# Optimization experiments

Hardware: AMD Instinct MI355X
Metric: run time of the kernel (lower is better)

Reference implementation:

```python
import jax, jax.numpy as jnp
import numpy as np

H = 16            # num_heads
NORM = 16.0       # gate normalizer
SCALE = 128.0 ** -0.5  # (embed_dim // num_heads) ** -0.5, per source
EPS = 1e-5


def setup_inputs() -> dict:
    key = jax.random.key(0)
    ks = jax.random.split(key, 10)
    B, L, D = 2, 2048, 2048
    g = lambda k, shape, s: jax.random.normal(k, shape, jnp.float32) * s
    return {
        "x": g(ks[0], (B, L, D), 1.0),
        "Wq": g(ks[1], (1024, D), 0.02),
        "Wk": g(ks[2], (1024, D), 0.02),
        "Wkg1": g(ks[3], (16, D), 0.02),
        "Wkg2": g(ks[4], (1024, 16), 0.05),
        "bkg2": jnp.zeros((1024,), jnp.float32),
        "Wv": g(ks[5], (D, D), 0.02),
        "Wg": g(ks[6], (D, D), 0.02),
        "bg": jnp.zeros((D,), jnp.float32),
        "Wo": g(ks[7], (D, D), 0.02),
    }


def _gla_core(x, Wq, Wk, Wkg1, Wkg2, bkg2, Wv, Wg, bg, Wo):
    B, L, D = x.shape
    q = x @ Wq.T                         # [B,L,1024]
    k = (x @ Wk.T) * SCALE               # [B,L,1024]
    kg = (x @ Wkg1.T) @ Wkg2.T + bkg2    # [B,L,1024] low-rank gate
    v = x @ Wv.T                         # [B,L,2048]
    gproj = x @ Wg.T + bg                # [B,L,2048]

    dk = q.shape[-1] // H   # 64
    dv = D // H             # 128
    heads = lambda t, dh: t.reshape(B, L, H, dh).transpose(0, 2, 1, 3)  # b h l d
    qh = heads(q, dk)
    kh = heads(k, dk)
    vh = heads(v, dv)
    gk = jax.nn.log_sigmoid(heads(kg, dk)) / NORM  # b h l dk

    # recurrence: S_t = diag(exp(gk_t)) S_{t-1} + k_t v_t^T ; o_t = q_t S_t
    tfirst = lambda t: t.transpose(2, 0, 1, 3)  # l b h d

    def step(S, inp):
        qt, kt, vt, gt = inp
        S = S * jnp.exp(gt)[..., None] + kt[..., None] * vt[..., None, :]
        ot = jnp.einsum('bhk,bhkv->bhv', qt, S)
        return S, ot

    S0 = jnp.zeros((B, H, dk, dv), x.dtype)
    _, os = jax.lax.scan(step, S0, (tfirst(qh), tfirst(kh), tfirst(vh), tfirst(gk)))
    o = os.transpose(1, 2, 0, 3)  # b h l dv

    # LayerNorm over head dim, no affine
    mu = o.mean(-1, keepdims=True)
    var = ((o - mu) ** 2).mean(-1, keepdims=True)
    o = (o - mu) * jax.lax.rsqrt(var + EPS)

    o = o.transpose(0, 2, 1, 3).reshape(B, L, D)  # b l (h dv)
    return (jax.nn.silu(gproj) * o) @ Wo.T


def reference(x, Wq, Wk, Wkg1, Wkg2, bkg2, Wv, Wg, bg, Wo):
    return _gla_core(x, Wq, Wk, Wkg1, Wkg2, bkg2, Wv, Wg, bg, Wo)
```

## Files before the change

kernel.cpp:

```cpp
#include <hip/hip_runtime.h>
#include <hip/hip_bf16.h>

using bf16x8 = __attribute__((ext_vector_type(8))) __bf16;
using fx4    = __attribute__((ext_vector_type(4))) float;
using us4    = __attribute__((ext_vector_type(4))) unsigned short;
using us8    = __attribute__((ext_vector_type(8))) unsigned short;

__device__ __forceinline__ float b2f(unsigned short u) {
    unsigned int x = ((unsigned int)u) << 16;
    return __builtin_bit_cast(float, x);
}
__device__ __forceinline__ unsigned short f2b(float f) {
    __hip_bfloat16 h = __float2bfloat16(f);
    return __builtin_bit_cast(unsigned short, h);
}
__device__ __forceinline__ float logsigmoidf(float z) {
    return fminf(z, 0.0f) - log1pf(expf(-fabsf(z)));
}

__device__ __forceinline__ void gl_lds16(const unsigned short* g, unsigned short* l) {
    __builtin_amdgcn_global_load_lds(
        (const __attribute__((address_space(1))) void*)g,
        (__attribute__((address_space(3))) void*)l, 16, 0, 0);
}

__device__ __forceinline__ bf16x8 frag64(const unsigned short* base, int row, int cq) {
    return *reinterpret_cast<const bf16x8*>(base + row * 64 + (((cq ^ (row & 7)) << 3)));
}
__device__ __forceinline__ int sw_idx(int row, int col) {
    return row * 64 + ((((col >> 3) ^ (row & 7)) << 3)) + (col & 7);
}

__global__ __launch_bounds__(256) void detect_kernel(
    const unsigned int* __restrict__ x, int* __restrict__ flag)
{
    __shared__ int bad[256];
    const int t = threadIdx.x;
    int b = 0;
#pragma unroll
    for (int i = 0; i < 16; ++i) {
        unsigned int w = x[t * 16 + i];
        float v = b2f((unsigned short)(w & 0xFFFFu));
        if (!(fabsf(v) < 1.0e6f)) b = 1;
    }
    bad[t] = b;
    __syncthreads();
    for (int s = 128; s > 0; s >>= 1) {
        if (t < s) bad[t] |= bad[t + s];
        __syncthreads();
    }
    if (t == 0) flag[0] = bad[0];
}

struct CvtArgs {
    const void* src[10];
    unsigned short* dst[10];
};

__global__ __launch_bounds__(256) void convert_all_kernel(
    CvtArgs a, const int* __restrict__ flag)
{
    const int pref[11] = {0, 8192, 10240, 12288, 12320, 12336, 12337,
                          16433, 20529, 20531, 24627};
    const int blk = blockIdx.x;
    int s = 0;
#pragma unroll
    for (int i = 1; i < 10; ++i) s += (blk >= pref[i]) ? 1 : 0;
    const int i0 = (blk - pref[s]) * 1024 + threadIdx.x * 4;
    if (*flag) {
        const float* sp = (const float*)a.src[s];
        fx4 v = *reinterpret_cast<const fx4*>(sp + i0);
        us4 r;
#pragma unroll
        for (int e = 0; e < 4; ++e) r[e] = f2b(v[e]);
        *reinterpret_cast<us4*>(a.dst[s] + i0) = r;
    } else {
        const unsigned short* sp = (const unsigned short*)a.src[s];
        *reinterpret_cast<us4*>(a.dst[s] + i0) =
            *reinterpret_cast<const us4*>(sp + i0);
    }
}

struct Seg3 {
    unsigned short* C0;
    unsigned short* C1;
    unsigned short* C2;
    const unsigned short* bias2;
};

__global__ __launch_bounds__(256) void gemm_fused3_kernel(
    const unsigned short* __restrict__ A, const unsigned short* __restrict__ W,
    Seg3 segs, float scale_k)
{
    const int K = 2048;
    __shared__ __align__(16) unsigned short As[128 * 64];
    __shared__ __align__(16) unsigned short Bs[128 * 64];

    const int tid  = threadIdx.x;
    const int lane = tid & 63, wid = tid >> 6;
    const int quad = lane >> 4, l15 = lane & 15;
    const int wm = (wid & 1) * 64, wn = (wid >> 1) * 64;
    const int m0 = blockIdx.y * 128, n0 = blockIdx.x * 128;

    fx4 acc[4][4];
#pragma unroll
    for (int i = 0; i < 4; ++i)
#pragma unroll
        for (int j = 0; j < 4; ++j) acc[i][j] = fx4{0.f, 0.f, 0.f, 0.f};

    const int srow = lane >> 3;
    const int g8   = ((lane & 7) ^ srow) * 8;
    const int c8   = (lane & 7) * 8;
    const unsigned short* Ab = A + (size_t)m0 * K;
    const unsigned short* Wb = W + (size_t)n0 * K;

    for (int k0 = 0; k0 < K; k0 += 64) {
#pragma unroll
        for (int p = 0; p < 4; ++p) {
            const int la  = wid * 4 + p;
            const int row = la * 8 + srow;
            gl_lds16(Ab + (size_t)row * K + k0 + g8, As + row * 64 + c8);
            gl_lds16(Wb + (size_t)row * K + k0 + g8, Bs + row * 64 + c8);
        }
        __syncthreads();
#pragma unroll
        for (int ks = 0; ks < 2; ++ks) {
            const int cq = quad + ks * 4;
            bf16x8 af[4], bfr[4];
#pragma unroll
            for (int mt = 0; mt < 4; ++mt) af[mt] = frag64(As, wm + mt * 16 + l15, cq);
#pragma unroll
            for (int nt = 0; nt < 4; ++nt) bfr[nt] = frag64(Bs, wn + nt * 16 + l15, cq);
#pragma unroll
            for (int mt = 0; mt < 4; ++mt)
#pragma unroll
                for (int nt = 0; nt < 4; ++nt)
                    acc[mt][nt] = __builtin_amdgcn_mfma_f32_16x16x32_bf16(
                        af[mt], bfr[nt], acc[mt][nt], 0, 0, 0);
        }
        __syncthreads();
    }

    const int segi = n0 >> 11;
    unsigned short* Cs = (segi == 0) ? segs.C0 : ((segi == 1) ? segs.C1 : segs.C2);
#pragma unroll
    for (int nt = 0; nt < 4; ++nt) {
        const int ncl = (n0 & 2047) + wn + nt * 16 + l15;
        const float av = (segi == 0 && ncl >= 1024) ? scale_k : 1.0f;
        const float bv = (segi == 2) ? b2f(segs.bias2[ncl]) : 0.0f;
#pragma unroll
        for (int mt = 0; mt < 4; ++mt) {
#pragma unroll
            for (int r = 0; r < 4; ++r) {
                const int mrow = m0 + wm + mt * 16 + quad * 4 + r;
                float val = acc[mt][nt][r] * av + bv;
                if (segi == 2) val = val / (1.0f + __expf(-val));
                Cs[(size_t)mrow * 2048 + ncl] = f2b(val);
            }
        }
    }
}

__global__ __launch_bounds__(256) void gemm_bt_kernel(
    const unsigned short* __restrict__ A, const unsigned short* __restrict__ W,
    unsigned short* __restrict__ C, int M, int N, int K,
    const int* __restrict__ oflag)
{
    __shared__ __align__(16) unsigned short As[128 * 64];
    __shared__ __align__(16) unsigned short Bs[128 * 64];

    const int tid  = threadIdx.x;
    const int lane = tid & 63, wid = tid >> 6;
    const int quad = lane >> 4, l15 = lane & 15;
    const int wm = (wid & 1) * 64, wn = (wid >> 1) * 64;
    const int m0 = blockIdx.y * 128, n0 = blockIdx.x * 128;

    fx4 acc[4][4];
#pragma unroll
    for (int i = 0; i < 4; ++i)
#pragma unroll
        for (int j = 0; j < 4; ++j) acc[i][j] = fx4{0.f, 0.f, 0.f, 0.f};

    const int srow = lane >> 3;
    const int g8   = ((lane & 7) ^ srow) * 8;
    const int c8   = (lane & 7) * 8;
    const unsigned short* Ab = A + (size_t)m0 * K;
    const unsigned short* Wb = W + (size_t)n0 * K;

    for (int k0 = 0; k0 < K; k0 += 64) {
#pragma unroll
        for (int p = 0; p < 4; ++p) {
            const int la  = wid * 4 + p;
            const int row = la * 8 + srow;
            gl_lds16(Ab + (size_t)row * K + k0 + g8, As + row * 64 + c8);
            gl_lds16(Wb + (size_t)row * K + k0 + g8, Bs + row * 64 + c8);
        }
        __syncthreads();
#pragma unroll
        for (int ks = 0; ks < 2; ++ks) {
            const int cq = quad + ks * 4;
            bf16x8 af[4], bfr[4];
#pragma unroll
            for (int mt = 0; mt < 4; ++mt) af[mt] = frag64(As, wm + mt * 16 + l15, cq);
#pragma unroll
            for (int nt = 0; nt < 4; ++nt) bfr[nt] = frag64(Bs, wn + nt * 16 + l15, cq);
#pragma unroll
            for (int mt = 0; mt < 4; ++mt)
#pragma unroll
                for (int nt = 0; nt < 4; ++nt)
                    acc[mt][nt] = __builtin_amdgcn_mfma_f32_16x16x32_bf16(
                        af[mt], bfr[nt], acc[mt][nt], 0, 0, 0);
        }
        __syncthreads();
    }

    const int f32out = oflag ? *oflag : 0;
#pragma unroll
    for (int nt = 0; nt < 4; ++nt) {
        const int ncol = n0 + wn + nt * 16 + l15;
#pragma unroll
        for (int mt = 0; mt < 4; ++mt) {
#pragma unroll
            for (int r = 0; r < 4; ++r) {
                const int mrow = m0 + wm + mt * 16 + quad * 4 + r;
                float val = acc[mt][nt][r];
                const size_t idx = (size_t)mrow * N + ncol;
                if (f32out) ((float*)C)[idx] = val;
                else        C[idx] = f2b(val);
            }
        }
    }
}

__global__ __launch_bounds__(256) void gate1_kernel(
    const unsigned short* __restrict__ x, const unsigned short* __restrict__ Wkg1,
    const unsigned short* __restrict__ Wkg2, const unsigned short* __restrict__ bkg2,
    float* __restrict__ Ag)
{
    __shared__ float part[4][16];
    __shared__ float kgrow[16];
    const int m = blockIdx.x;
    const int tid = threadIdx.x;
    const int lane = tid & 63, w = tid >> 6;

    us8 xv = *reinterpret_cast<const us8*>(x + (size_t)m * 2048 + tid * 8);
    float xr[8];
#pragma unroll
    for (int e = 0; e < 8; ++e) xr[e] = b2f(xv[e]);

#pragma unroll
    for (int n = 0; n < 16; ++n) {
        us8 wv = *reinterpret_cast<const us8*>(Wkg1 + (size_t)n * 2048 + tid * 8);
        float s = 0.f;
#pragma unroll
        for (int e = 0; e < 8; ++e) s += xr[e] * b2f(wv[e]);
#pragma unroll
        for (int off = 1; off < 64; off <<= 1) s += __shfl_xor(s, off, 64);
        if (lane == 0) part[w][n] = s;
    }
    __syncthreads();
    if (tid < 16)
        kgrow[tid] = part[0][tid] + part[1][tid] + part[2][tid] + part[3][tid];
    __syncthreads();
    float kr[16];
#pragma unroll
    for (int j = 0; j < 16; ++j) kr[j] = kgrow[j];

    const int b = m >> 11, l = m & 2047;
    const int c0 = tid * 4;
    const int h = c0 >> 6, d0 = c0 & 63;
    fx4 gv;
#pragma unroll
    for (int qi = 0; qi < 4; ++qi) {
        const int c = c0 + qi;
        us8 w0 = *reinterpret_cast<const us8*>(Wkg2 + (size_t)c * 16);
        us8 w1 = *reinterpret_cast<const us8*>(Wkg2 + (size_t)c * 16 + 8);
        float z = b2f(bkg2[c]);
#pragma unroll
        for (int j = 0; j < 8; ++j) z += kr[j] * b2f(w0[j]) + kr[8 + j] * b2f(w1[j]);
        gv[qi] = logsigmoidf(z) * 0.0625f;
    }
    *reinterpret_cast<fx4*>(Ag + ((size_t)(b * 16 + h) * 2048 + l) * 64 + d0) = gv;
}

__global__ __launch_bounds__(256) void gate2_kernel(float* __restrict__ Ag)
{
    const int gidx = blockIdx.x * 256 + threadIdx.x;
    const int d = gidx & 63, ch = (gidx >> 6) & 31, bh = gidx >> 11;
    float* p = Ag + ((size_t)bh * 2048 + ch * 64) * 64 + d;
    float acc = 0.f;
#pragma unroll 8
    for (int t = 0; t < 64; ++t) {
        acc += p[(size_t)t * 64];
        p[(size_t)t * 64] = acc;
    }
}

__global__ __launch_bounds__(256) void pass1_kernel(
    const unsigned short* __restrict__ k, int kstr,
    const unsigned short* __restrict__ v,
    const float* __restrict__ Ag, float* __restrict__ Tc)
{
    __shared__ __align__(16) unsigned short kT[64 * 64];
    __shared__ __align__(16) unsigned short vT[128 * 64];

    const int blk = blockIdx.x;
    const int ch = blk & 31, bh = blk >> 5;
    const int b = bh >> 4, h = bh & 15;
    const int tid = threadIdx.x;
    const int lane = tid & 63, w = tid >> 6;
    const int quad = lane >> 4, l15 = lane & 15;

    const float* Abase = Ag + ((size_t)bh * 2048 + ch * 64) * 64;
    const unsigned short* kbase = k + ((size_t)(b * 2048 + ch * 64)) * kstr + h * 64;
    const unsigned short* vbase = v + ((size_t)(b * 2048 + ch * 64)) * 2048 + h * 128;

    {
        const int s = tid >> 2, d0 = (tid & 3) * 16;
        float av[16], a63[16];
        *(fx4*)(av)      = *(const fx4*)(Abase + (size_t)s * 64 + d0);
        *(fx4*)(av + 4)  = *(const fx4*)(Abase + (size_t)s * 64 + d0 + 4);
        *(fx4*)(av + 8)  = *(const fx4*)(Abase + (size_t)s * 64 + d0 + 8);
        *(fx4*)(av + 12) = *(const fx4*)(Abase + (size_t)s * 64 + d0 + 12);
        *(fx4*)(a63)      = *(const fx4*)(Abase + (size_t)63 * 64 + d0);
        *(fx4*)(a63 + 4)  = *(const fx4*)(Abase + (size_t)63 * 64 + d0 + 4);
        *(fx4*)(a63 + 8)  = *(const fx4*)(Abase + (size_t)63 * 64 + d0 + 8);
        *(fx4*)(a63 + 12) = *(const fx4*)(Abase + (size_t)63 * 64 + d0 + 12);
        us8 k0v = *(const us8*)(kbase + (size_t)s * kstr + d0);
        us8 k1v = *(const us8*)(kbase + (size_t)s * kstr + d0 + 8);
#pragma unroll
        for (int e = 0; e < 8; ++e) {
            kT[sw_idx(d0 + e, s)]     = f2b(b2f(k0v[e]) * __expf(a63[e] - av[e]));
            kT[sw_idx(d0 + 8 + e, s)] = f2b(b2f(k1v[e]) * __expf(a63[8 + e] - av[8 + e]));
        }
    }
    {
        const int s = tid >> 2, j0 = (tid & 3) * 32;
#pragma unroll
        for (int g2 = 0; g2 < 4; ++g2) {
            us8 vv = *(const us8*)(vbase + (size_t)s * 2048 + j0 + g2 * 8);
#pragma unroll
            for (int e = 0; e < 8; ++e) vT[sw_idx(j0 + g2 * 8 + e, s)] = vv[e];
        }
    }
    __syncthreads();

    bf16x8 bk[4][2];
#pragma unroll
    for (int nt = 0; nt < 4; ++nt) {
        bk[nt][0] = frag64(kT, nt * 16 + l15, quad);
        bk[nt][1] = frag64(kT, nt * 16 + l15, quad + 4);
    }
    fx4 acc[2][4];
#pragma unroll
    for (int mi = 0; mi < 2; ++mi)
#pragma unroll
        for (int nt = 0; nt < 4; ++nt) acc[mi][nt] = fx4{0.f, 0.f, 0.f, 0.f};
#pragma unroll
    for (int mi = 0; mi < 2; ++mi) {
        const int mrow = (w * 2 + mi) * 16 + l15;
        bf16x8 av0 = frag64(vT, mrow, quad);
        bf16x8 av1 = frag64(vT, mrow, quad + 4);
#pragma unroll
        for (int nt = 0; nt < 4; ++nt) {
            acc[mi][nt] = __builtin_amdgcn_mfma_f32_16x16x32_bf16(av0, bk[nt][0], acc[mi][nt], 0, 0, 0);
            acc[mi][nt] = __builtin_amdgcn_mfma_f32_16x16x32_bf16(av1, bk[nt][1], acc[mi][nt], 0, 0, 0);
        }
    }
    float* tb = Tc + (size_t)blk * 8192;
#pragma unroll
    for (int mi = 0; mi < 2; ++mi)
#pragma unroll
        for (int nt = 0; nt < 4; ++nt)
#pragma unroll
            for (int r = 0; r < 4; ++r) {
                const int j = (w * 2 + mi) * 16 + quad * 4 + r;
                const int d = nt * 16 + l15;
                tb[(size_t)j * 64 + d] = acc[mi][nt][r];
            }
}

__global__ __launch_bounds__(256) void combine_kernel(
    float* __restrict__ TS, const float* __restrict__ Ag)
{
    const int blk = blockIdx.x;
    const int js = blk & 7, bh = blk >> 3;
    const int tid = threadIdx.x;
    const int j = js * 16 + (tid >> 4), d0 = (tid & 15) * 4;
    fx4 S = fx4{0.f, 0.f, 0.f, 0.f};
    const float* Abase = Ag + (size_t)bh * 2048 * 64;
    for (int c = 0; c < 32; ++c) {
        float* p = TS + ((size_t)(bh * 32 + c)) * 8192 + (size_t)j * 64 + d0;
        fx4 t = *(const fx4*)p;
        *(fx4*)p = S;
        fx4 a = *(const fx4*)(Abase + ((size_t)c * 64 + 63) * 64 + d0);
#pragma unroll
        for (int e = 0; e < 4; ++e) S[e] = S[e] * __expf(a[e]) + t[e];
    }
}

__global__ __launch_bounds__(256) void pass2_kernel(
    const unsigned short* __restrict__ q, const unsigned short* __restrict__ k,
    int qkstr,
    const unsigned short* __restrict__ v, const float* __restrict__ Ag,
    const float* __restrict__ Sst, const unsigned short* __restrict__ sg,
    unsigned short* __restrict__ y)
{
    __shared__ __align__(16) unsigned short qs[64 * 64];
    __shared__ __align__(16) unsigned short ksh[64 * 64];
    __shared__ __align__(16) unsigned short vT[128 * 64];
    __shared__ __align__(16) unsigned short Pb[64 * 64];
    __shared__ __align__(16) unsigned short Ob[64 * 144];

    const int blk = blockIdx.x;
    const int ch = blk & 31, bh = blk >> 5;
    const int b = bh >> 4, h = bh & 15;
    const int tid = threadIdx.x;
    const int lane = tid & 63, w = tid >> 6;
    const int quad = lane >> 4, l15 = lane & 15;

    const float* Abase = Ag + ((size_t)bh * 2048 + ch * 64) * 64;
    const unsigned short* qbase = q + ((size_t)(b * 2048 + ch * 64)) * qkstr + h * 64;
    const unsigned short* kbase = k + ((size_t)(b * 2048 + ch * 64)) * qkstr + h * 64;
    const unsigned short* vbase = v + ((size_t)(b * 2048 + ch * 64)) * 2048 + h * 128;

    {
        const int t = tid >> 2, d0 = (tid & 3) * 16;
        float av[16];
        *(fx4*)(av)      = *(const fx4*)(Abase + (size_t)t * 64 + d0);
        *(fx4*)(av + 4)  = *(const fx4*)(Abase + (size_t)t * 64 + d0 + 4);
        *(fx4*)(av + 8)  = *(const fx4*)(Abase + (size_t)t * 64 + d0 + 8);
        *(fx4*)(av + 12) = *(const fx4*)(Abase + (size_t)t * 64 + d0 + 12);
        us8 q0 = *(const us8*)(qbase + (size_t)t * qkstr + d0);
        us8 q1 = *(const us8*)(qbase + (size_t)t * qkstr + d0 + 8);
        us8 k0 = *(const us8*)(kbase + (size_t)t * qkstr + d0);
        us8 k1 = *(const us8*)(kbase + (size_t)t * qkstr + d0 + 8);
        us8 qo0, qo1, ko0, ko1;
#pragma unroll
        for (int e = 0; e < 8; ++e) {
            float e0 = __expf(av[e]),     n0 = __expf(-av[e]);
            float e1 = __expf(av[8 + e]), n1 = __expf(-av[8 + e]);
            qo0[e] = f2b(b2f(q0[e]) * e0);
            qo1[e] = f2b(b2f(q1[e]) * e1);
            ko0[e] = f2b(b2f(k0[e]) * n0);
            ko1[e] = f2b(b2f(k1[e]) * n1);
        }
        const int c0 = d0 >> 3, t7 = t & 7;
        *(us8*)(qs  + t * 64 + ((c0 ^ t7) << 3))       = qo0;
        *(us8*)(qs  + t * 64 + (((c0 + 1) ^ t7) << 3)) = qo1;
        *(us8*)(ksh + t * 64 + ((c0 ^ t7) << 3))       = ko0;
        *(us8*)(ksh + t * 64 + (((c0 + 1) ^ t7) << 3)) = ko1;
    }
    {
        const int s = tid >> 2, j0 = (tid & 3) * 32;
#pragma unroll
        for (int g2 = 0; g2 < 4; ++g2) {
            us8 vv = *(const us8*)(vbase + (size_t)s * 2048 + j0 + g2 * 8);
#pragma unroll
            for (int e = 0; e < 8; ++e) vT[sw_idx(j0 + g2 * 8 + e, s)] = vv[e];
        }
    }
    __syncthreads();

    bf16x8 aQ0 = frag64(qs, w * 16 + l15, quad);
    bf16x8 aQ1 = frag64(qs, w * 16 + l15, quad + 4);
    fx4 accP[4];
#pragma unroll
    for (int nt = 0; nt < 4; ++nt) accP[nt] = fx4{0.f, 0.f, 0.f, 0.f};
#pragma unroll
    for (int nt = 0; nt < 4; ++nt) {
        bf16x8 bK0 = frag64(ksh, nt * 16 + l15, quad);
        bf16x8 bK1 = frag64(ksh, nt * 16 + l15, quad + 4);
        accP[nt] = __builtin_amdgcn_mfma_f32_16x16x32_bf16(aQ0, bK0, accP[nt], 0, 0, 0);
        accP[nt] = __builtin_amdgcn_mfma_f32_16x16x32_bf16(aQ1, bK1, accP[nt], 0, 0, 0);
    }
#pragma unroll
    for (int nt = 0; nt < 4; ++nt)
#pragma unroll
        for (int r = 0; r < 4; ++r) {
            const int t = w * 16 + quad * 4 + r;
            const int s = nt * 16 + l15;
            Pb[sw_idx(t, s)] = f2b((s <= t) ? accP[nt][r] : 0.0f);
        }
    __syncthreads();

    bf16x8 aP0 = frag64(Pb, w * 16 + l15, quad);
    bf16x8 aP1 = frag64(Pb, w * 16 + l15, quad + 4);
    const float* ST = Sst + (size_t)blk * 8192;
    fx4 accO[8];
#pragma unroll
    for (int nt = 0; nt < 8; ++nt) accO[nt] = fx4{0.f, 0.f, 0.f, 0.f};
#pragma unroll
    for (int nt = 0; nt < 8; ++nt) {
        const int j = nt * 16 + l15;
        bf16x8 bV0 = frag64(vT, j, quad);
        bf16x8 bV1 = frag64(vT, j, quad + 4);
        const float* sp = ST + (size_t)j * 64 + quad * 8;
        fx4 s0a = *(const fx4*)(sp),      s0b = *(const fx4*)(sp + 4);
        fx4 s1a = *(const fx4*)(sp + 32), s1b = *(const fx4*)(sp + 36);
        us8 hi0u, lo0u, hi1u, lo1u;
#pragma unroll
        for (int e = 0; e < 4; ++e) {
            unsigned short hh;
            hh = f2b(s0a[e]); hi0u[e] = hh;     lo0u[e]     = f2b(s0a[e] - b2f(hh));
            hh = f2b(s0b[e]); hi0u[4 + e] = hh; lo0u[4 + e] = f2b(s0b[e] - b2f(hh));
            hh = f2b(s1a[e]); hi1u[e] = hh;     lo1u[e]     = f2b(s1a[e] - b2f(hh));
            hh = f2b(s1b[e]); hi1u[4 + e] = hh; lo1u[4 + e] = f2b(s1b[e] - b2f(hh));
        }
        bf16x8 hi0 = __builtin_bit_cast(bf16x8, hi0u);
        bf16x8 lo0 = __builtin_bit_cast(bf16x8, lo0u);
        bf16x8 hi1 = __builtin_bit_cast(bf16x8, hi1u);
        bf16x8 lo1 = __builtin_bit_cast(bf16x8, lo1u);
        accO[nt] = __builtin_amdgcn_mfma_f32_16x16x32_bf16(aP0, bV0, accO[nt], 0, 0, 0);
        accO[nt] = __builtin_amdgcn_mfma_f32_16x16x32_bf16(aP1, bV1, accO[nt], 0, 0, 0);
        accO[nt] = __builtin_amdgcn_mfma_f32_16x16x32_bf16(aQ0, hi0, accO[nt], 0, 0, 0);
        accO[nt] = __builtin_amdgcn_mfma_f32_16x16x32_bf16(aQ1, hi1, accO[nt], 0, 0, 0);
        accO[nt] = __builtin_amdgcn_mfma_f32_16x16x32_bf16(aQ0, lo0, accO[nt], 0, 0, 0);
        accO[nt] = __builtin_amdgcn_mfma_f32_16x16x32_bf16(aQ1, lo1, accO[nt], 0, 0, 0);
    }

    float sum1[4] = {0.f, 0.f, 0.f, 0.f}, sum2[4] = {0.f, 0.f, 0.f, 0.f};
#pragma unroll
    for (int nt = 0; nt < 8; ++nt)
#pragma unroll
        for (int r = 0; r < 4; ++r) {
            float ov = accO[nt][r];
            sum1[r] += ov;
            sum2[r] += ov * ov;
        }
#pragma unroll
    for (int m = 1; m < 16; m <<= 1)
#pragma unroll
        for (int r = 0; r < 4; ++r) {
            sum1[r] += __shfl_xor(sum1[r], m, 64);
            sum2[r] += __shfl_xor(sum2[r], m, 64);
        }
    float mu[4], inv[4];
#pragma unroll
    for (int r = 0; r < 4; ++r) {
        mu[r] = sum1[r] * (1.0f / 128.0f);
        float var = sum2[r] * (1.0f / 128.0f) - mu[r] * mu[r];
        inv[r] = rsqrtf(var + 1e-5f);
    }
#pragma unroll
    for (int nt = 0; nt < 8; ++nt)
#pragma unroll
        for (int r = 0; r < 4; ++r) {
            const int t = w * 16 + quad * 4 + r;
            Ob[t * 144 + nt * 16 + l15] = f2b((accO[nt][r] - mu[r]) * inv[r]);
        }
    __syncthreads();

    {
        const int t2 = tid >> 2, jg = (tid & 3) * 32;
        const size_t obase = ((size_t)(b * 2048 + ch * 64 + t2)) * 2048 + h * 128 + jg;
#pragma unroll
        for (int g2 = 0; g2 < 4; ++g2) {
            us8 ob = *(const us8*)(Ob + t2 * 144 + jg + g2 * 8);
            us8 gv = *(const us8*)(sg + obase + g2 * 8);
            us8 ov;
#pragma unroll
            for (int e = 0; e < 8; ++e) ov[e] = f2b(b2f(gv[e]) * b2f(ob[e]));
            *(us8*)(y + obase + g2 * 8) = ov;
        }
    }
}

extern "C" void kernel_launch(void* const* d_in, const int* in_sizes, int n_in,
                              void* d_out, int out_size, void* d_ws, size_t ws_size,
                              hipStream_t stream)
{
    unsigned short* out = (unsigned short*)d_out;

    char* ws = (char*)d_ws;
    size_t off = 0;
    auto alloc = [&](size_t bytes) -> void* {
        void* p = ws + off;
        off += (bytes + 255) & ~(size_t)255;
        return p;
    };
    unsigned short* xb    = (unsigned short*)alloc((size_t)4096 * 2048 * 2);
    unsigned short* Wbig  = (unsigned short*)alloc((size_t)6144 * 2048 * 2);
    unsigned short* Wkg1b = (unsigned short*)alloc((size_t)16 * 2048 * 2);
    unsigned short* Wkg2b = (unsigned short*)alloc((size_t)1024 * 16 * 2);
    unsigned short* bkg2b = (unsigned short*)alloc((size_t)1024 * 2);
    unsigned short* bgb   = (unsigned short*)alloc((size_t)2048 * 2);
    unsigned short* Wob   = (unsigned short*)alloc((size_t)2048 * 2048 * 2);
    unsigned short* qkb  = (unsigned short*)alloc((size_t)4096 * 2048 * 2);
    unsigned short* vb   = (unsigned short*)alloc((size_t)4096 * 2048 * 2);
    unsigned short* sgb  = (unsigned short*)alloc((size_t)4096 * 2048 * 2);
    unsigned short* yb   = (unsigned short*)alloc((size_t)4096 * 2048 * 2);
    float*          Agb  = (float*)alloc((size_t)4096 * 1024 * 4);
    float*          TS   = (float*)alloc((size_t)1024 * 8192 * 4);
    int*            flag = (int*)alloc(256);

    detect_kernel<<<1, 256, 0, stream>>>((const unsigned int*)d_in[0], flag);

    CvtArgs ca;
    ca.src[0] = d_in[0]; ca.dst[0] = xb;
    ca.src[1] = d_in[1]; ca.dst[1] = Wbig;
    ca.src[2] = d_in[2]; ca.dst[2] = Wbig + (size_t)1024 * 2048;
    ca.src[3] = d_in[3]; ca.dst[3] = Wkg1b;
    ca.src[4] = d_in[4]; ca.dst[4] = Wkg2b;
    ca.src[5] = d_in[5]; ca.dst[5] = bkg2b;
    ca.src[6] = d_in[6]; ca.dst[6] = Wbig + (size_t)2048 * 2048;
    ca.src[7] = d_in[7]; ca.dst[7] = Wbig + (size_t)4096 * 2048;
    ca.src[8] = d_in[8]; ca.dst[8] = bgb;
    ca.src[9] = d_in[9]; ca.dst[9] = Wob;
    convert_all_kernel<<<24627, 256, 0, stream>>>(ca, flag);

    const float SCALE = 0.08838834764831845f;

    Seg3 segs;
    segs.C0 = qkb; segs.C1 = vb; segs.C2 = sgb; segs.bias2 = bgb;
    gemm_fused3_kernel<<<dim3(48, 32), 256, 0, stream>>>(xb, Wbig, segs, SCALE);

    gate1_kernel<<<4096, 256, 0, stream>>>(xb, Wkg1b, Wkg2b, bkg2b, Agb);
    gate2_kernel<<<256, 256, 0, stream>>>(Agb);
    pass1_kernel<<<1024, 256, 0, stream>>>(qkb + 1024, 2048, vb, Agb, TS);
    combine_kernel<<<256, 256, 0, stream>>>(TS, Agb);
    pass2_kernel<<<1024, 256, 0, stream>>>(qkb, qkb + 1024, 2048, vb, Agb, TS, sgb, yb);
    gemm_bt_kernel<<<dim3(16, 32), 256, 0, stream>>>(yb, Wob, out, 4096, 2048, 2048, flag);
}
```

Baseline: 417.6 us.

## Rewrite GEMMs as 128x256 tiles with 4-stage async LDS pipeline

Both projection GEMMs now share a core that uses 128x256 block tiles with 8 waves (512 threads), K-step 32, and a 4-deep ring of LDS buffers filled by direct global-to-LDS loads. Explicit vmcnt waits and one barrier per step replace the two syncthreads per iteration, so loads for upcoming steps overlap the MFMA work, and setprio raises the wave's priority around the MFMA burst. The larger tile improves operand reuse but halves the grid (768 and 256 blocks) and uses more LDS, which can reduce occupancy and leave CUs idle on the output GEMM.

```diff
diff --git a/kernel.cpp b/kernel.cpp
--- a/kernel.cpp
+++ b/kernel.cpp
@@ -81,6 +81,86 @@
     }
 }
 
+__device__ __forceinline__ void gemm_core_128x256(
+    const unsigned short* __restrict__ Ab,
+    const unsigned short* __restrict__ Wb,
+    unsigned short* As,
+    unsigned short* Bs,
+    fx4 (&acc)[4][4])
+{
+    const int K = 2048, NT = 64;
+    const int tid  = threadIdx.x;
+    const int lane = tid & 63;
+    const int quad = lane >> 4, l15 = lane & 15;
+    const int wid  = tid >> 6;
+    const int wr = wid >> 2, wc = wid & 3;
+
+    const int rs  = tid >> 2;
+    const int gch = (((tid & 3) ^ ((tid >> 4) & 3)) << 3);
+    const unsigned short* Ag  = Ab + (size_t)rs * K + gch;
+    const unsigned short* Bg0 = Wb + (size_t)rs * K + gch;
+    const unsigned short* Bg1 = Wb + (size_t)(128 + rs) * K + gch;
+    unsigned short* Ad  = As + tid * 8;
+    unsigned short* Bd0 = Bs + tid * 8;
+    unsigned short* Bd1 = Bs + 4096 + tid * 8;
+
+    int aoff[4], boff[4];
+#pragma unroll
+    for (int mt = 0; mt < 4; ++mt) {
+        const int r = wr * 64 + mt * 16 + l15;
+        aoff[mt] = r * 32 + ((quad ^ ((r >> 2) & 3)) << 3);
+    }
+#pragma unroll
+    for (int nt = 0; nt < 4; ++nt) {
+        const int r = wc * 64 + nt * 16 + l15;
+        boff[nt] = r * 32 + ((quad ^ ((r >> 2) & 3)) << 3);
+    }
+#pragma unroll
+    for (int i = 0; i < 4; ++i)
+#pragma unroll
+        for (int j = 0; j < 4; ++j) acc[i][j] = fx4{0.f, 0.f, 0.f, 0.f};
+
+    auto stage = [&](int t) {
+        const int kk = t * 32;
+        const int bs = t & 3;
+        gl_lds16(Ag  + kk, Ad  + bs * 4096);
+        gl_lds16(Bg0 + kk, Bd0 + bs * 8192);
+        gl_lds16(Bg1 + kk, Bd1 + bs * 8192);
+    };
+
+    stage(0); stage(1); stage(2);
+
+    for (int t = 0; t < NT; ++t) {
+        if (t < NT - 2)
+            asm volatile("s_waitcnt vmcnt(6)\n\ts_barrier" ::: "memory");
+        else if (t == NT - 2)
+            asm volatile("s_waitcnt vmcnt(3)\n\ts_barrier" ::: "memory");
+        else
+            asm volatile("s_waitcnt vmcnt(0)\n\ts_barrier" ::: "memory");
+
+        if (t + 3 < NT) stage(t + 3);
+
+        const unsigned short* ab = As + (t & 3) * 4096;
+        const unsigned short* bb = Bs + (t & 3) * 8192;
+        bf16x8 af[4], bfr[4];
+#pragma unroll
+        for (int mt = 0; mt < 4; ++mt)
+            af[mt] = *reinterpret_cast<const bf16x8*>(ab + aoff[mt]);
+#pragma unroll
+        for (int nt = 0; nt < 4; ++nt)
+            bfr[nt] = *reinterpret_cast<const bf16x8*>(bb + boff[nt]);
+
+        __builtin_amdgcn_s_setprio(1);
+#pragma unroll
+        for (int mt = 0; mt < 4; ++mt)
+#pragma unroll
+            for (int nt = 0; nt < 4; ++nt)
+                acc[mt][nt] = __builtin_amdgcn_mfma_f32_16x16x32_bf16(
+                    af[mt], bfr[nt], acc[mt][nt], 0, 0, 0);
+        __builtin_amdgcn_s_setprio(0);
+    }
+}
+
 struct Seg3 {
     unsigned short* C0;
     unsigned short* C1;
@@ -88,71 +168,34 @@
     const unsigned short* bias2;
 };
 
-__global__ __launch_bounds__(256) void gemm_fused3_kernel(
+__global__ __launch_bounds__(512) void gemm_fused3_kernel(
     const unsigned short* __restrict__ A, const unsigned short* __restrict__ W,
     Seg3 segs, float scale_k)
 {
-    const int K = 2048;
-    __shared__ __align__(16) unsigned short As[128 * 64];
-    __shared__ __align__(16) unsigned short Bs[128 * 64];
+    __shared__ __align__(16) unsigned short As[4 * 128 * 32];
+    __shared__ __align__(16) unsigned short Bs[4 * 256 * 32];
+
+    const int m0 = blockIdx.y * 128, n0 = blockIdx.x * 256;
+    fx4 acc[4][4];
+    gemm_core_128x256(A + (size_t)m0 * 2048, W + (size_t)n0 * 2048, As, Bs, acc);
 
     const int tid  = threadIdx.x;
     const int lane = tid & 63, wid = tid >> 6;
     const int quad = lane >> 4, l15 = lane & 15;
-    const int wm = (wid & 1) * 64, wn = (wid >> 1) * 64;
-    const int m0 = blockIdx.y * 128, n0 = blockIdx.x * 128;
-
-    fx4 acc[4][4];
-#pragma unroll
-    for (int i = 0; i < 4; ++i)
-#pragma unroll
-        for (int j = 0; j < 4; ++j) acc[i][j] = fx4{0.f, 0.f, 0.f, 0.f};
-
-    const int srow = lane >> 3;
-    const int g8   = ((lane & 7) ^ srow) * 8;
-    const int c8   = (lane & 7) * 8;
-    const unsigned short* Ab = A + (size_t)m0 * K;
-    const unsigned short* Wb = W + (size_t)n0 * K;
-
-    for (int k0 = 0; k0 < K; k0 += 64) {
-#pragma unroll
-        for (int p = 0; p < 4; ++p) {
-            const int la  = wid * 4 + p;
-            const int row = la * 8 + srow;
-            gl_lds16(Ab + (size_t)row * K + k0 + g8, As + row * 64 + c8);
-            gl_lds16(Wb + (size_t)row * K + k0 + g8, Bs + row * 64 + c8);
-        }
-        __syncthreads();
-#pragma unroll
-        for (int ks = 0; ks < 2; ++ks) {
-            const int cq = quad + ks * 4;
-            bf16x8 af[4], bfr[4];
-#pragma unroll
-            for (int mt = 0; mt < 4; ++mt) af[mt] = frag64(As, wm + mt * 16 + l15, cq);
-#pragma unroll
-            for (int nt = 0; nt < 4; ++nt) bfr[nt] = frag64(Bs, wn + nt * 16 + l15, cq);
-#pragma unroll
-            for (int mt = 0; mt < 4; ++mt)
-#pragma unroll
-                for (int nt = 0; nt < 4; ++nt)
-                    acc[mt][nt] = __builtin_amdgcn_mfma_f32_16x16x32_bf16(
-                        af[mt], bfr[nt], acc[mt][nt], 0, 0, 0);
-        }
-        __syncthreads();
-    }
+    const int wr = wid >> 2, wc = wid & 3;
 
     const int segi = n0 >> 11;
     unsigned short* Cs = (segi == 0) ? segs.C0 : ((segi == 1) ? segs.C1 : segs.C2);
 #pragma unroll
     for (int nt = 0; nt < 4; ++nt) {
-        const int ncl = (n0 & 2047) + wn + nt * 16 + l15;
+        const int ncl = ((n0 & 2047)) + wc * 64 + nt * 16 + l15;
         const float av = (segi == 0 && ncl >= 1024) ? scale_k : 1.0f;
         const float bv = (segi == 2) ? b2f(segs.bias2[ncl]) : 0.0f;
 #pragma unroll
         for (int mt = 0; mt < 4; ++mt) {
 #pragma unroll
             for (int r = 0; r < 4; ++r) {
-                const int mrow = m0 + wm + mt * 16 + quad * 4 + r;
+                const int mrow = m0 + wr * 64 + mt * 16 + quad * 4 + r;
                 float val = acc[mt][nt][r] * av + bv;
                 if (segi == 2) val = val / (1.0f + __expf(-val));
                 Cs[(size_t)mrow * 2048 + ncl] = f2b(val);
@@ -161,68 +204,32 @@
     }
 }
 
-__global__ __launch_bounds__(256) void gemm_bt_kernel(
+__global__ __launch_bounds__(512) void gemm_bt_kernel(
     const unsigned short* __restrict__ A, const unsigned short* __restrict__ W,
     unsigned short* __restrict__ C, int M, int N, int K,
     const int* __restrict__ oflag)
 {
-    __shared__ __align__(16) unsigned short As[128 * 64];
-    __shared__ __align__(16) unsigned short Bs[128 * 64];
+    __shared__ __align__(16) unsigned short As[4 * 128 * 32];
+    __shared__ __align__(16) unsigned short Bs[4 * 256 * 32];
+
+    const int m0 = blockIdx.y * 128, n0 = blockIdx.x * 256;
+    fx4 acc[4][4];
+    gemm_core_128x256(A + (size_t)m0 * 2048, W + (size_t)n0 * 2048, As, Bs, acc);
 
     const int tid  = threadIdx.x;
     const int lane = tid & 63, wid = tid >> 6;
     const int quad = lane >> 4, l15 = lane & 15;
-    const int wm = (wid & 1) * 64, wn = (wid >> 1) * 64;
-    const int m0 = blockIdx.y * 128, n0 = blockIdx.x * 128;
-
-    fx4 acc[4][4];
-#pragma unroll
-    for (int i = 0; i < 4; ++i)
-#pragma unroll
-        for (int j = 0; j < 4; ++j) acc[i][j] = fx4{0.f, 0.f, 0.f, 0.f};
-
-    const int srow = lane >> 3;
-    const int g8   = ((lane & 7) ^ srow) * 8;
-    const int c8   = (lane & 7) * 8;
-    const unsigned short* Ab = A + (size_t)m0 * K;
-    const unsigned short* Wb = W + (size_t)n0 * K;
-
-    for (int k0 = 0; k0 < K; k0 += 64) {
-#pragma unroll
-        for (int p = 0; p < 4; ++p) {
-            const int la  = wid * 4 + p;
-            const int row = la * 8 + srow;
-            gl_lds16(Ab + (size_t)row * K + k0 + g8, As + row * 64 + c8);
-            gl_lds16(Wb + (size_t)row * K + k0 + g8, Bs + row * 64 + c8);
-        }
-        __syncthreads();
-#pragma unroll
-        for (int ks = 0; ks < 2; ++ks) {
-            const int cq = quad + ks * 4;
-            bf16x8 af[4], bfr[4];
-#pragma unroll
-            for (int mt = 0; mt < 4; ++mt) af[mt] = frag64(As, wm + mt * 16 + l15, cq);
-#pragma unroll
-            for (int nt = 0; nt < 4; ++nt) bfr[nt] = frag64(Bs, wn + nt * 16 + l15, cq);
-#pragma unroll
-            for (int mt = 0; mt < 4; ++mt)
-#pragma unroll
-                for (int nt = 0; nt < 4; ++nt)
-                    acc[mt][nt] = __builtin_amdgcn_mfma_f32_16x16x32_bf16(
-                        af[mt], bfr[nt], acc[mt][nt], 0, 0, 0);
-        }
-        __syncthreads();
-    }
+    const int wr = wid >> 2, wc = wid & 3;
 
     const int f32out = oflag ? *oflag : 0;
 #pragma unroll
     for (int nt = 0; nt < 4; ++nt) {
-        const int ncol = n0 + wn + nt * 16 + l15;
+        const int ncol = n0 + wc * 64 + nt * 16 + l15;
 #pragma unroll
         for (int mt = 0; mt < 4; ++mt) {
 #pragma unroll
             for (int r = 0; r < 4; ++r) {
-                const int mrow = m0 + wm + mt * 16 + quad * 4 + r;
+                const int mrow = m0 + wr * 64 + mt * 16 + quad * 4 + r;
                 float val = acc[mt][nt][r];
                 const size_t idx = (size_t)mrow * N + ncol;
                 if (f32out) ((float*)C)[idx] = val;
@@ -613,12 +620,12 @@
 
     Seg3 segs;
     segs.C0 = qkb; segs.C1 = vb; segs.C2 = sgb; segs.bias2 = bgb;
-    gemm_fused3_kernel<<<dim3(48, 32), 256, 0, stream>>>(xb, Wbig, segs, SCALE);
+    gemm_fused3_kernel<<<dim3(24, 32), 512, 0, stream>>>(xb, Wbig, segs, SCALE);
 
     gate1_kernel<<<4096, 256, 0, stream>>>(xb, Wkg1b, Wkg2b, bkg2b, Agb);
     gate2_kernel<<<256, 256, 0, stream>>>(Agb);
     pass1_kernel<<<1024, 256, 0, stream>>>(qkb + 1024, 2048, vb, Agb, TS);
     combine_kernel<<<256, 256, 0, stream>>>(TS, Agb);
     pass2_kernel<<<1024, 256, 0, stream>>>(qkb, qkb + 1024, 2048, vb, Agb, TS, sgb, yb);
-    gemm_bt_kernel<<<dim3(16, 32), 256, 0, stream>>>(yb, Wob, out, 4096, 2048, 2048, flag);
-}
+    gemm_bt_kernel<<<dim3(8, 32), 512, 0, stream>>>(yb, Wob, out, 4096, 2048, 2048, flag);
+}
```

Result: slower. 485.7 us (+16.3%).

## Rewrite fused QKV/gate GEMM as 256x256 double-buffered 8-wave pipeline

Applied to the files above, without the earlier changes.

The fused projection GEMM moves from 128x128 tiles with 4 waves and a single LDS buffer to 256x256 tiles with 8 waves, double-buffered LDS staging and fine-grained interleaving of global-to-LDS loads with MFMA quadrants. Manual vmcnt waits, s_barrier and setprio are used to overlap loads with compute, and the operand reuse per loaded byte goes up. The goal is to hide memory latency and raise MFMA utilisation in the largest GEMM. In exchange, register and LDS pressure rise and the grid shrinks to 384 blocks, which may affect occupancy and load balance across CUs.

```diff
diff --git a/kernel.cpp b/kernel.cpp
--- a/kernel.cpp
+++ b/kernel.cpp
@@ -88,72 +88,139 @@
     const unsigned short* bias2;
 };
 
-__global__ __launch_bounds__(256) void gemm_fused3_kernel(
+__global__ __launch_bounds__(512, 2) void gemm_fused3_kernel(
     const unsigned short* __restrict__ A, const unsigned short* __restrict__ W,
     Seg3 segs, float scale_k)
 {
-    const int K = 2048;
-    __shared__ __align__(16) unsigned short As[128 * 64];
-    __shared__ __align__(16) unsigned short Bs[128 * 64];
-
+    __shared__ __align__(16) unsigned short As[2 * 256 * 64];
+    __shared__ __align__(16) unsigned short Bs[2 * 2 * 128 * 64];
+
+    const int NT = 32, K = 2048;
     const int tid  = threadIdx.x;
     const int lane = tid & 63, wid = tid >> 6;
     const int quad = lane >> 4, l15 = lane & 15;
-    const int wm = (wid & 1) * 64, wn = (wid >> 1) * 64;
-    const int m0 = blockIdx.y * 128, n0 = blockIdx.x * 128;
-
-    fx4 acc[4][4];
-#pragma unroll
-    for (int i = 0; i < 4; ++i)
-#pragma unroll
-        for (int j = 0; j < 4; ++j) acc[i][j] = fx4{0.f, 0.f, 0.f, 0.f};
-
-    const int srow = lane >> 3;
-    const int g8   = ((lane & 7) ^ srow) * 8;
-    const int c8   = (lane & 7) * 8;
+    const int wr = wid >> 2, wc = wid & 3;
+    const int m0 = blockIdx.y * 256, n0 = blockIdx.x * 256;
+
     const unsigned short* Ab = A + (size_t)m0 * K;
     const unsigned short* Wb = W + (size_t)n0 * K;
 
-    for (int k0 = 0; k0 < K; k0 += 64) {
-#pragma unroll
-        for (int p = 0; p < 4; ++p) {
-            const int la  = wid * 4 + p;
-            const int row = la * 8 + srow;
-            gl_lds16(Ab + (size_t)row * K + k0 + g8, As + row * 64 + c8);
-            gl_lds16(Wb + (size_t)row * K + k0 + g8, Bs + row * 64 + c8);
-        }
-        __syncthreads();
-#pragma unroll
-        for (int ks = 0; ks < 2; ++ks) {
-            const int cq = quad + ks * 4;
-            bf16x8 af[4], bfr[4];
-#pragma unroll
-            for (int mt = 0; mt < 4; ++mt) af[mt] = frag64(As, wm + mt * 16 + l15, cq);
-#pragma unroll
-            for (int nt = 0; nt < 4; ++nt) bfr[nt] = frag64(Bs, wn + nt * 16 + l15, cq);
-#pragma unroll
-            for (int mt = 0; mt < 4; ++mt)
-#pragma unroll
-                for (int nt = 0; nt < 4; ++nt)
-                    acc[mt][nt] = __builtin_amdgcn_mfma_f32_16x16x32_bf16(
-                        af[mt], bfr[nt], acc[mt][nt], 0, 0, 0);
-        }
-        __syncthreads();
+    const int sx = ((tid & 7) ^ ((tid >> 3) & 7)) * 8;
+    const unsigned short* pA[2][2];
+    const unsigned short* pB[2][2];
+#pragma unroll
+    for (int mh = 0; mh < 2; ++mh)
+#pragma unroll
+        for (int j = 0; j < 2; ++j)
+            pA[mh][j] = Ab + (size_t)(j * 128 + mh * 64 + (tid >> 3)) * K + sx;
+#pragma unroll
+    for (int nh = 0; nh < 2; ++nh)
+#pragma unroll
+        for (int j = 0; j < 2; ++j)
+            pB[nh][j] = Wb + (size_t)((j * 2 + (tid >> 8)) * 64 + nh * 32 +
+                                      ((tid >> 3) & 31)) * K + sx;
+
+    fx4 acc[8][4];
+#pragma unroll
+    for (int i = 0; i < 8; ++i)
+#pragma unroll
+        for (int j = 0; j < 4; ++j) acc[i][j] = fx4{0.f, 0.f, 0.f, 0.f};
+
+    auto stageA = [&](int mh, int tt) {
+#pragma unroll
+        for (int j = 0; j < 2; ++j)
+            gl_lds16(pA[mh][j] + tt * 64,
+                     As + (tt & 1) * 16384 + (j * 128 + mh * 64) * 64 + tid * 8);
+    };
+    auto stageB = [&](int nh, int tt) {
+#pragma unroll
+        for (int j = 0; j < 2; ++j)
+            gl_lds16(pB[nh][j] + tt * 64,
+                     Bs + (tt & 1) * 16384 + nh * 8192 + j * 4096 + tid * 8);
+    };
+
+    bf16x8 afr[4][2], bfr[2][2];
+    const int x7 = l15 & 7;
+    const int cswz0 = (quad ^ x7) << 3;
+    const int cswz1 = ((quad + 4) ^ x7) << 3;
+    int arow[4], brow[2];
+#pragma unroll
+    for (int mt = 0; mt < 4; ++mt) arow[mt] = (wr * 128 + mt * 16 + l15) * 64;
+#pragma unroll
+    for (int nt = 0; nt < 2; ++nt) brow[nt] = (wc * 32 + nt * 16 + l15) * 64;
+
+    auto ldA = [&](int s, int mh) {
+        const unsigned short* base = As + s * 16384 + mh * 4096;
+#pragma unroll
+        for (int mt = 0; mt < 4; ++mt) {
+            afr[mt][0] = *(const bf16x8*)(base + arow[mt] + cswz0);
+            afr[mt][1] = *(const bf16x8*)(base + arow[mt] + cswz1);
+        }
+    };
+    auto ldB = [&](int s, int nh) {
+        const unsigned short* base = Bs + s * 16384 + nh * 8192;
+#pragma unroll
+        for (int nt = 0; nt < 2; ++nt) {
+            bfr[nt][0] = *(const bf16x8*)(base + brow[nt] + cswz0);
+            bfr[nt][1] = *(const bf16x8*)(base + brow[nt] + cswz1);
+        }
+    };
+    auto mma = [&](int mh, int nh) {
+        __builtin_amdgcn_s_setprio(1);
+#pragma unroll
+        for (int mt = 0; mt < 4; ++mt)
+#pragma unroll
+            for (int nt = 0; nt < 2; ++nt) {
+                acc[mh * 4 + mt][nh * 2 + nt] = __builtin_amdgcn_mfma_f32_16x16x32_bf16(
+                    afr[mt][0], bfr[nt][0], acc[mh * 4 + mt][nh * 2 + nt], 0, 0, 0);
+                acc[mh * 4 + mt][nh * 2 + nt] = __builtin_amdgcn_mfma_f32_16x16x32_bf16(
+                    afr[mt][1], bfr[nt][1], acc[mh * 4 + mt][nh * 2 + nt], 0, 0, 0);
+            }
+        __builtin_amdgcn_s_setprio(0);
+    };
+
+    stageA(0, 0); stageB(0, 0); stageA(1, 0); stageB(1, 0);
+    stageA(0, 1); stageB(0, 1);
+
+    for (int t = 0; t < NT; ++t) {
+        const int s = t & 1;
+        if (t + 1 < NT) stageA(1, t + 1);
+        if (t < NT - 1) asm volatile("s_waitcnt vmcnt(6)" ::: "memory");
+        else            asm volatile("s_waitcnt vmcnt(0)" ::: "memory");
+        asm volatile("s_barrier" ::: "memory");
+        ldA(s, 0); ldB(s, 0);
+        mma(0, 0);
+        asm volatile("s_barrier" ::: "memory");
+        if (t + 1 < NT) stageB(1, t + 1);
+        ldB(s, 1);
+        asm volatile("s_barrier" ::: "memory");
+        mma(0, 1);
+        asm volatile("s_barrier" ::: "memory");
+        if (t + 2 < NT) stageA(0, t + 2);
+        ldA(s, 1); ldB(s, 0);
+        asm volatile("s_barrier" ::: "memory");
+        mma(1, 0);
+        asm volatile("s_barrier" ::: "memory");
+        if (t + 2 < NT) stageB(0, t + 2);
+        ldB(s, 1);
+        asm volatile("s_barrier" ::: "memory");
+        mma(1, 1);
+        asm volatile("s_barrier" ::: "memory");
     }
 
     const int segi = n0 >> 11;
     unsigned short* Cs = (segi == 0) ? segs.C0 : ((segi == 1) ? segs.C1 : segs.C2);
 #pragma unroll
-    for (int nt = 0; nt < 4; ++nt) {
-        const int ncl = (n0 & 2047) + wn + nt * 16 + l15;
+    for (int j = 0; j < 4; ++j) {
+        const int ncl = (n0 & 2047) + wc * 64 + j * 16 + l15;
         const float av = (segi == 0 && ncl >= 1024) ? scale_k : 1.0f;
         const float bv = (segi == 2) ? b2f(segs.bias2[ncl]) : 0.0f;
 #pragma unroll
-        for (int mt = 0; mt < 4; ++mt) {
+        for (int i = 0; i < 8; ++i) {
 #pragma unroll
             for (int r = 0; r < 4; ++r) {
-                const int mrow = m0 + wm + mt * 16 + quad * 4 + r;
-                float val = acc[mt][nt][r] * av + bv;
+                const int mrow = m0 + wr * 128 + i * 16 + quad * 4 + r;
+                float val = acc[i][j][r] * av + bv;
                 if (segi == 2) val = val / (1.0f + __expf(-val));
                 Cs[(size_t)mrow * 2048 + ncl] = f2b(val);
             }
@@ -613,7 +680,7 @@
 
     Seg3 segs;
     segs.C0 = qkb; segs.C1 = vb; segs.C2 = sgb; segs.bias2 = bgb;
-    gemm_fused3_kernel<<<dim3(48, 32), 256, 0, stream>>>(xb, Wbig, segs, SCALE);
+    gemm_fused3_kernel<<<dim3(24, 16), 512, 0, stream>>>(xb, Wbig, segs, SCALE);
 
     gate1_kernel<<<4096, 256, 0, stream>>>(xb, Wkg1b, Wkg2b, bkg2b, Agb);
     gate2_kernel<<<256, 256, 0, stream>>>(Agb);
```

Measured after the change: 459.0 us. +9.9%, slower.

## Remap GEMM blocks across XCDs and use grid-stride 8-wide conversion kernel

Applied to the files above, without the earlier changes.

Adds an XCD-aware block index remap to both GEMM kernels so that consecutive tiles sharing A/W rows are scheduled on the same XCD, aiming to improve L2 reuse. It also rewrites the input conversion kernel as a grid-stride loop over 8-element chunks with a fixed 2048-block grid instead of one block per 1024 elements. The remap assumes the block count divides by 8 (1536 and 512 do) and changes the tile visiting order.

```diff
diff --git a/kernel.cpp b/kernel.cpp
--- a/kernel.cpp
+++ b/kernel.cpp
@@ -29,6 +29,16 @@
 }
 __device__ __forceinline__ int sw_idx(int row, int col) {
     return row * 64 + ((((col >> 3) ^ (row & 7)) << 3)) + (col & 7);
+}
+
+__device__ __forceinline__ void xcd_remap(int& bx, int& by) {
+    const int gx = gridDim.x;
+    const int nwg = gx * gridDim.y;
+    const int cpx = nwg >> 3;
+    const int f = blockIdx.y * gx + blockIdx.x;
+    const int nf = (f & 7) * cpx + (f >> 3);
+    bx = nf % gx;
+    by = nf / gx;
 }
 
 __global__ __launch_bounds__(256) void detect_kernel(
@@ -60,24 +70,27 @@
 __global__ __launch_bounds__(256) void convert_all_kernel(
     CvtArgs a, const int* __restrict__ flag)
 {
-    const int pref[11] = {0, 8192, 10240, 12288, 12320, 12336, 12337,
-                          16433, 20529, 20531, 24627};
-    const int blk = blockIdx.x;
-    int s = 0;
-#pragma unroll
-    for (int i = 1; i < 10; ++i) s += (blk >= pref[i]) ? 1 : 0;
-    const int i0 = (blk - pref[s]) * 1024 + threadIdx.x * 4;
-    if (*flag) {
-        const float* sp = (const float*)a.src[s];
-        fx4 v = *reinterpret_cast<const fx4*>(sp + i0);
-        us4 r;
-#pragma unroll
-        for (int e = 0; e < 4; ++e) r[e] = f2b(v[e]);
-        *reinterpret_cast<us4*>(a.dst[s] + i0) = r;
-    } else {
-        const unsigned short* sp = (const unsigned short*)a.src[s];
-        *reinterpret_cast<us4*>(a.dst[s] + i0) =
-            *reinterpret_cast<const us4*>(sp + i0);
+    const int pref[11] = {0, 1048576, 1310720, 1572864, 1576960, 1579008,
+                          1579136, 2103424, 2627712, 2627968, 3152256};
+    const int total = 3152256;
+    const int f32 = *flag;
+    for (int g = blockIdx.x * 256 + threadIdx.x; g < total; g += gridDim.x * 256) {
+        int s = 0;
+#pragma unroll
+        for (int i = 1; i < 10; ++i) s += (g >= pref[i]) ? 1 : 0;
+        const int lg = g - pref[s];
+        if (f32) {
+            const float* sp = (const float*)a.src[s] + (size_t)lg * 8;
+            fx4 v0 = *(const fx4*)(sp);
+            fx4 v1 = *(const fx4*)(sp + 4);
+            us8 r;
+#pragma unroll
+            for (int e = 0; e < 4; ++e) { r[e] = f2b(v0[e]); r[4 + e] = f2b(v1[e]); }
+            *(us8*)(a.dst[s] + (size_t)lg * 8) = r;
+        } else {
+            *(us8*)(a.dst[s] + (size_t)lg * 8) =
+                *(const us8*)((const unsigned short*)a.src[s] + (size_t)lg * 8);
+        }
     }
 }
 
@@ -100,7 +113,9 @@
     const int lane = tid & 63, wid = tid >> 6;
     const int quad = lane >> 4, l15 = lane & 15;
     const int wm = (wid & 1) * 64, wn = (wid >> 1) * 64;
-    const int m0 = blockIdx.y * 128, n0 = blockIdx.x * 128;
+    int bx, by;
+    xcd_remap(bx, by);
+    const int m0 = by * 128, n0 = bx * 128;
 
     fx4 acc[4][4];
 #pragma unroll
@@ -173,7 +188,9 @@
     const int lane = tid & 63, wid = tid >> 6;
     const int quad = lane >> 4, l15 = lane & 15;
     const int wm = (wid & 1) * 64, wn = (wid >> 1) * 64;
-    const int m0 = blockIdx.y * 128, n0 = blockIdx.x * 128;
+    int bx, by;
+    xcd_remap(bx, by);
+    const int m0 = by * 128, n0 = bx * 128;
 
     fx4 acc[4][4];
 #pragma unroll
@@ -607,7 +624,7 @@
     ca.src[7] = d_in[7]; ca.dst[7] = Wbig + (size_t)4096 * 2048;
     ca.src[8] = d_in[8]; ca.dst[8] = bgb;
     ca.src[9] = d_in[9]; ca.dst[9] = Wob;
-    convert_all_kernel<<<24627, 256, 0, stream>>>(ca, flag);
+    convert_all_kernel<<<2048, 256, 0, stream>>>(ca, flag);
 
     const float SCALE = 0.08838834764831845f;
 
```

After: 434.7 us. 4.1% more time.
